# Performance work log

Measured on AMD Instinct MI355X. Metric: run time of the kernel, lower is better.

Reference implementation:

```python
import jax, jax.numpy as jnp
import numpy as np

K = 5          # kernel_size per dim
DIM = 2        # pseudo-coordinate dim
S = 2 ** DIM   # number of contributing knots for degree-1 B-spline
N = 50000
E = 800000
IN_C = 32
OUT_C = 64
NUM_LAYERS = 2
KPROD = K ** DIM  # 25 kernel weight matrices


def setup_inputs() -> dict:
    key = jax.random.key(0)
    ks = jax.random.split(key, 16)
    x = jax.random.normal(ks[0], (N, IN_C), dtype=jnp.float32)
    edge_index = jax.random.randint(ks[1], (2, E), 0, N, dtype=jnp.int64)
    edge_attr = jax.random.uniform(ks[2], (E, DIM), dtype=jnp.float32)
    inp = {"x": x, "edge_index": edge_index, "edge_attr": edge_attr}
    # SplineConv params per layer: spline weight [KPROD, in, out], root weight [in, out], bias [out]
    cin = IN_C
    for l in range(NUM_LAYERS):
        scale = 1.0 / np.sqrt(cin * S)
        inp[f"w{l}"] = jax.random.normal(ks[3 + 3 * l], (KPROD, cin, OUT_C), dtype=jnp.float32) * scale
        inp[f"root{l}"] = jax.random.normal(ks[4 + 3 * l], (cin, OUT_C), dtype=jnp.float32) / np.sqrt(cin)
        inp[f"b{l}"] = jnp.zeros((OUT_C,), dtype=jnp.float32)
        cin = OUT_C
    fin = IN_C + NUM_LAYERS * OUT_C  # 160, cat=True
    inp["fw"] = jax.random.normal(ks[10], (fin, OUT_C), dtype=jnp.float32) / np.sqrt(fin)
    inp["fb"] = jnp.zeros((OUT_C,), dtype=jnp.float32)
    return inp


def spline_basis(edge_attr):
    # degree-1 open B-spline over pseudo-coords in [0,1)
    v = edge_attr * (K - 1)                       # [E, DIM]
    bot = jnp.floor(v)
    frac = v - bot                                # [E, DIM]
    bits = ((jnp.arange(S)[:, None] >> jnp.arange(DIM)[None, :]) & 1)  # [S, DIM]
    bitsf = bits.astype(edge_attr.dtype)
    # basis_s = prod_d (frac_d if bit else 1-frac_d)
    basis = jnp.prod(bitsf[None] * frac[:, None, :] + (1.0 - bitsf[None]) * (1.0 - frac[:, None, :]), axis=-1)  # [E, S]
    kidx = jnp.clip(bot[:, None, :].astype(jnp.int32) + bits[None], 0, K - 1)  # [E, S, DIM]
    strides = (K ** jnp.arange(DIM)).astype(jnp.int32)
    widx = jnp.sum(kidx * strides[None, None, :], axis=-1)  # [E, S] in [0, KPROD)
    return basis, widx


def spline_conv(x, src, dst, basis, widx, w, root, b):
    # per-node, per-kernel transforms, then edge gather + basis weighting
    y = jnp.einsum('ni,kio->nko', x, w)           # [N, KPROD, out]
    msg = jnp.sum(basis[:, :, None] * y[src[:, None], widx], axis=1)  # [E, out]
    agg = jax.ops.segment_sum(msg, dst, num_segments=x.shape[0])
    deg = jax.ops.segment_sum(jnp.ones((src.shape[0],), x.dtype), dst, num_segments=x.shape[0])
    agg = agg / jnp.maximum(deg, 1.0)[:, None]    # mean aggregation
    return agg + x @ root + b


def reference(x, edge_index, edge_attr, w0, root0, b0, w1, root1, b1, fw, fb):
    src = edge_index[0].astype(jnp.int32)
    dst = edge_index[1].astype(jnp.int32)
    basis, widx = spline_basis(edge_attr)
    xs = [x]
    for w, root, b in ((w0, root0, b0), (w1, root1, b1)):
        xs.append(jax.nn.relu(spline_conv(xs[-1], src, dst, basis, widx, w, root, b)))
    h = jnp.concatenate(xs, axis=-1)              # cat=True -> [N, in + L*out]
    # dropout p=0.0 / eval mode -> identity
    return h @ fw + fb
```

## Files before the change

### kernel.cpp

```cpp
#include <hip/hip_runtime.h>
#include <hip/hip_bf16.h>
#include <hip/hip_fp16.h>


typedef __attribute__((ext_vector_type(8))) _Float16 f16x8;
typedef __attribute__((ext_vector_type(4))) _Float16 f16x4;
typedef __attribute__((ext_vector_type(4))) float f32x4;

constexpr int NN = 50000;
constexpr int EE = 800000;
constexpr int CHUNK = 256;
constexpr int EB = EE / 256;
static_assert(EE % 256 == 0, "prep grid assumes exact divisibility");
constexpr int ELIST_LEN = EE + 16 * CHUNK;
constexpr int NBLK_EDGE = ELIST_LEN / CHUNK;
constexpr int RT_BLK = (NN + 63) / 64;

__global__ __launch_bounds__(256) void detect_init(
    const long long* __restrict__ eidx, int* __restrict__ flag,
    int* __restrict__ degi) {
  if (blockIdx.x == 0 && threadIdx.x < 64) {
    long long v = eidx[threadIdx.x];
    bool ok = (v >= 0) && (v < (long long)NN);
    unsigned long long m = __ballot(ok);
    if (threadIdx.x == 0) flag[0] = (m == ~0ull) ? 1 : 0;
  }
  const int i = blockIdx.x * 256 + threadIdx.x;
  if (i < NN) degi[i] = 0;
}

constexpr int F2H_LEN8 = NN * 32 / 8;
constexpr int F2H_BLK = (F2H_LEN8 + 255) / 256;
constexpr int CW32_BLK = 4 * 16;
constexpr int CW64_BLK = 8 * 16;
constexpr int CFW_BLK = (64 * 160) / 256;
constexpr int CRT0_BLK = (64 * 32) / 256;
constexpr int CRT1_BLK = (64 * 64) / 256;
constexpr int CONV_BLK = F2H_BLK + CW32_BLK + CW64_BLK + CFW_BLK + CRT0_BLK + CRT1_BLK;

template <int IN>
__device__ __forceinline__ void conv_w_body(
    const float* __restrict__ w, _Float16* __restrict__ wcell, int c, int o) {
  constexpr int K = 4 * IN;
  constexpr int RS = K * 2;
  constexpr int OPR = K / 8;
  const int bx = c & 3, by = c >> 2;
  const int n = o / OPR;
  const int k0 = (o - n * OPR) * 8;
  const int ks = k0 >> 5;
  const int g2 = (k0 & 31) >> 3;
  const int s = (IN == 64) ? (ks & 3) : ks;
  const int i0 = ((IN == 64) ? (ks >> 2) * 32 : 0) + g2 * 8;
  const int kk = (bx + (s & 1)) + 5 * (by + (s >> 1));
  const float* wp = w + ((size_t)kk * IN + i0) * 64 + n;
  f16x8 v;
#pragma unroll
  for (int j = 0; j < 8; ++j) v[j] = (_Float16)wp[(size_t)j * 64];
  const int byte = n * RS + ((k0 * 2) ^ ((n & 15) << 4));
  *reinterpret_cast<f16x8*>(
      reinterpret_cast<char*>(wcell) + (size_t)c * (RS * 64) + byte) = v;
}

__global__ __launch_bounds__(256) void prep_conv(
    const void* __restrict__ eidx, const float* __restrict__ attr,
    const int* __restrict__ flag,
    int* __restrict__ src, int* __restrict__ dst, int* __restrict__ rankE,
    int* __restrict__ degi, int* __restrict__ bhT,
    const float* __restrict__ x0, const float* __restrict__ w0,
    const float* __restrict__ w1, const float* __restrict__ fw,
    const float* __restrict__ root0, const float* __restrict__ root1,
    _Float16* __restrict__ xh0, _Float16* __restrict__ wc0,
    _Float16* __restrict__ wc1, _Float16* __restrict__ fwT,
    _Float16* __restrict__ rt0T, _Float16* __restrict__ rt1T) {
  __shared__ int wc[4][16];
  const int tid = threadIdx.x;
  if (blockIdx.x < EB) {
    const int e = blockIdx.x * 256 + tid;
    int s, d;
    if (flag[0]) {
      s = (int)((const long long*)eidx)[e];
      d = (int)((const long long*)eidx)[EE + e];
    } else {
      s = ((const int*)eidx)[e];
      d = ((const int*)eidx)[EE + e];
    }
    src[e] = s;
    dst[e] = d;
    rankE[e] = atomicAdd(&degi[d], 1);
    const float v0 = attr[2 * e] * 4.0f, v1 = attr[2 * e + 1] * 4.0f;
    const int bx = min(max((int)floorf(v0), 0), 3);
    const int by = min(max((int)floorf(v1), 0), 3);
    const int c = bx + 4 * by;
    const int wave = tid >> 6, lane = tid & 63;
#pragma unroll
    for (int k = 0; k < 16; ++k) {
      unsigned long long mm = __ballot(c == k);
      if (lane == k) wc[wave][k] = __popcll(mm);
    }
    __syncthreads();
    if (tid < 16)
      bhT[tid * EB + blockIdx.x] = wc[0][tid] + wc[1][tid] + wc[2][tid] + wc[3][tid];
    return;
  }
  const int b = blockIdx.x - EB;
  if (b < F2H_BLK) {
    const int i = b * 256 + tid;
    if (i >= F2H_LEN8) return;
    const float4 a = reinterpret_cast<const float4*>(x0)[i * 2];
    const float4 bb = reinterpret_cast<const float4*>(x0)[i * 2 + 1];
    f16x8 v = {(_Float16)a.x, (_Float16)a.y, (_Float16)a.z, (_Float16)a.w,
               (_Float16)bb.x, (_Float16)bb.y, (_Float16)bb.z, (_Float16)bb.w};
    reinterpret_cast<f16x8*>(xh0)[i] = v;
  } else if (b < F2H_BLK + CW32_BLK) {
    const int r = b - F2H_BLK;
    conv_w_body<32>(w0, wc0, r >> 2, (r & 3) * 256 + tid);
  } else if (b < F2H_BLK + CW32_BLK + CW64_BLK) {
    const int r = b - F2H_BLK - CW32_BLK;
    conv_w_body<64>(w1, wc1, r >> 3, (r & 7) * 256 + tid);
  } else if (b < F2H_BLK + CW32_BLK + CW64_BLK + CFW_BLK) {
    const int i = (b - F2H_BLK - CW32_BLK - CW64_BLK) * 256 + tid;
    const int n = i / 160, k = i - n * 160;
    fwT[i] = (_Float16)fw[k * 64 + n];
  } else if (b < F2H_BLK + CW32_BLK + CW64_BLK + CFW_BLK + CRT0_BLK) {
    const int i = (b - F2H_BLK - CW32_BLK - CW64_BLK - CFW_BLK) * 256 + tid;
    const int n = i / 32, k = i - n * 32;
    rt0T[i] = (_Float16)root0[k * 64 + n];
  } else {
    const int i = (b - F2H_BLK - CW32_BLK - CW64_BLK - CFW_BLK - CRT0_BLK) * 256 + tid;
    const int n = i / 64, k = i - n * 64;
    rt1T[i] = (_Float16)root1[k * 64 + n];
  }
}

__global__ __launch_bounds__(1024) void scan_fused(
    const int* __restrict__ bhT, int* __restrict__ blkbaseT,
    int* __restrict__ chunkcell, int2* __restrict__ posrcS,
    const int* __restrict__ degi, int* __restrict__ dstbase) {
  const int wave = threadIdx.x >> 6, lane = threadIdx.x & 63;
  if (blockIdx.x == 0) {
    constexpr int CH = (EB + 63) / 64;
    __shared__ int ofs_s[16];
    __shared__ int tot_s[16];
    int v[CH];
#pragma unroll
    for (int ch = 0; ch < CH; ++ch) {
      const int b = ch * 64 + lane;
      v[ch] = (b < EB) ? bhT[wave * EB + b] : 0;
    }
    {
      int sum = 0;
#pragma unroll
      for (int ch = 0; ch < CH; ++ch) sum += v[ch];
#pragma unroll
      for (int off = 32; off > 0; off >>= 1) sum += __shfl_down(sum, off);
      if (lane == 0) tot_s[wave] = sum;
    }
    __syncthreads();
    if (threadIdx.x == 0) {
      int t = 0;
      for (int c = 0; c < 16; ++c) {
        ofs_s[c] = t;
        t += ((tot_s[c] + CHUNK - 1) / CHUNK) * CHUNK;
      }
    }
    __syncthreads();
    {
      const int nch = (tot_s[wave] + CHUNK - 1) / CHUNK;
      const int cb = ofs_s[wave] / CHUNK;
      for (int i = lane; i < nch; i += 64) chunkcell[cb + i] = wave;
      if (wave == 15) {
        const int totch = cb + nch;
        for (int i = totch + lane; i < NBLK_EDGE; i += 64) chunkcell[i] = -1;
      }
    }
    {
      const int startp = ofs_s[wave] + tot_s[wave];
      const int endp = ofs_s[wave] + ((tot_s[wave] + CHUNK - 1) / CHUNK) * CHUNK;
      for (int p = startp + lane; p < endp; p += 64) posrcS[p] = make_int2(-1, 0);
    }
    int running = ofs_s[wave];
#pragma unroll
    for (int ch = 0; ch < CH; ++ch) {
      int inc = v[ch];
#pragma unroll
      for (int off = 1; off < 64; off <<= 1) {
        int n = __shfl_up(inc, off);
        if (lane >= off) inc += n;
      }
      const int b = ch * 64 + lane;
      if (b < EB) blkbaseT[wave * EB + b] = running + inc - v[ch];
      running += __shfl(inc, 63);
    }
  } else {
    constexpr int SEG = NN / 16;
    constexpr int CH = (SEG + 63) / 64;
    __shared__ int wofs[16];
    const int nbase = wave * SEG;
    int v[CH];
#pragma unroll
    for (int ch = 0; ch < CH; ++ch) {
      const int i = ch * 64 + lane;
      v[ch] = (i < SEG) ? degi[nbase + i] : 0;
    }
    {
      int sum = 0;
#pragma unroll
      for (int ch = 0; ch < CH; ++ch) sum += v[ch];
#pragma unroll
      for (int off = 32; off > 0; off >>= 1) sum += __shfl_down(sum, off);
      if (lane == 0) wofs[wave] = sum;
    }
    __syncthreads();
    if (threadIdx.x == 0) {
      int t = 0;
      for (int w2 = 0; w2 < 16; ++w2) { int tv = wofs[w2]; wofs[w2] = t; t += tv; }
    }
    __syncthreads();
    int running = wofs[wave];
#pragma unroll
    for (int ch = 0; ch < CH; ++ch) {
      int inc = v[ch];
#pragma unroll
      for (int off = 1; off < 64; off <<= 1) {
        int n = __shfl_up(inc, off);
        if (lane >= off) inc += n;
      }
      const int i = ch * 64 + lane;
      if (i < SEG) dstbase[nbase + i] = running + inc - v[ch];
      running += __shfl(inc, 63);
    }
  }
}

__global__ __launch_bounds__(256) void scatter_edges(
    const float* __restrict__ attr, const int* __restrict__ blkbaseT,
    const int* __restrict__ srcArr, const int* __restrict__ dstArr,
    const int* __restrict__ rankE, const int* __restrict__ dstbase,
    int2* __restrict__ posrcS, f16x4* __restrict__ basS) {
  __shared__ int wc[4][16];
  __shared__ int bs[4][16];
  const int tid = threadIdx.x;
  const int e = blockIdx.x * 256 + tid;
  const float v0 = attr[2 * e] * 4.0f, v1 = attr[2 * e + 1] * 4.0f;
  const float fl0 = floorf(v0), fl1 = floorf(v1);
  const float fr0 = v0 - fl0, fr1 = v1 - fl1;
  const int bx = min(max((int)fl0, 0), 3);
  const int by = min(max((int)fl1, 0), 3);
  const int c = bx + 4 * by;
  const f16x4 bq = {(_Float16)((1.0f - fr0) * (1.0f - fr1)),
                    (_Float16)(fr0 * (1.0f - fr1)),
                    (_Float16)((1.0f - fr0) * fr1),
                    (_Float16)(fr0 * fr1)};
  const int wave = tid >> 6, lane = tid & 63;
  int rank = 0;
#pragma unroll
  for (int k = 0; k < 16; ++k) {
    unsigned long long mm = __ballot(c == k);
    if (k == c) rank = __popcll(mm & ((1ull << lane) - 1ull));
    if (lane == k) wc[wave][k] = __popcll(mm);
  }
  const int mypos = dstbase[dstArr[e]] + rankE[e];
  __syncthreads();
  if (tid < 16) {
    int running = blkbaseT[tid * EB + blockIdx.x];
#pragma unroll
    for (int w = 0; w < 4; ++w) { bs[w][tid] = running; running += wc[w][tid]; }
  }
  __syncthreads();
  const int p = bs[wave][c] + rank;
  posrcS[p] = make_int2(srcArr[e], mypos);
  basS[p] = bq;
}

template <int IN, bool TWOPASS>
__global__ __launch_bounds__(256) void edge_root(
    const _Float16* __restrict__ xh, const _Float16* __restrict__ wcell,
    const int* __restrict__ chunkcell,
    const int2* __restrict__ posrcS, const f16x4* __restrict__ basS,
    const _Float16* __restrict__ rootT, const float* __restrict__ bias,
    _Float16* __restrict__ rth,
    unsigned char* __restrict__ msg, float* __restrict__ agg) {
  constexpr int K = 4 * IN;
  constexpr int KSTEPS = K / 32;
  constexpr int RS = K * 2;
  constexpr int OPR = K / 8;
  constexpr int TILES = CHUNK / 64;
  constexpr int NCH = (IN == 64) ? 2 : 1;
  __shared__ f16x8 Wt[64 * OPR];
  const int tid = threadIdx.x;
  const int lane = tid & 63;
  const int wave = tid >> 6;
  const int g = lane >> 4, m = lane & 15;
  if (blockIdx.x >= NBLK_EDGE) {
    constexpr int KS = IN / 32;
    const int base = (blockIdx.x - NBLK_EDGE) * 64 + wave * 16;
    if (base >= NN) return;
    f16x8 bf[KS][4];
#pragma unroll
    for (int ks = 0; ks < KS; ++ks)
#pragma unroll
      for (int nt = 0; nt < 4; ++nt)
        bf[ks][nt] = *reinterpret_cast<const f16x8*>(
            rootT + (size_t)(nt * 16 + m) * IN + ks * 32 + g * 8);
    const int row = base + m;
    f16x8 a[KS];
#pragma unroll
    for (int ks = 0; ks < KS; ++ks)
      a[ks] = *reinterpret_cast<const f16x8*>(xh + (size_t)row * IN + ks * 32 + g * 8);
    f32x4 acc[4];
#pragma unroll
    for (int nt = 0; nt < 4; ++nt) {
      const float fv = bias[nt * 16 + m];
      acc[nt] = (f32x4){fv, fv, fv, fv};
    }
#pragma unroll
    for (int ks = 0; ks < KS; ++ks)
#pragma unroll
      for (int nt = 0; nt < 4; ++nt)
        acc[nt] = __builtin_amdgcn_mfma_f32_16x16x32_f16(a[ks], bf[ks][nt], acc[nt], 0, 0, 0);
#pragma unroll
    for (int r = 0; r < 4; ++r) {
      const int node = base + g * 4 + r;
      f16x4 pv = {(_Float16)acc[0][r], (_Float16)acc[1][r],
                  (_Float16)acc[2][r], (_Float16)acc[3][r]};
      *reinterpret_cast<f16x4*>(rth + (size_t)node * 64 + m * 4) = pv;
    }
    return;
  }
  const int c = chunkcell[blockIdx.x];
  if (c < 0) return;
  const int base = blockIdx.x * CHUNK;
  const int wbase = base + wave * (CHUNK / 4);
  int2 sp_t[TILES];
  f16x4 bas_t[TILES];
#pragma unroll
  for (int t = 0; t < TILES; ++t) sp_t[t] = posrcS[wbase + t * 16 + m];
#pragma unroll
  for (int t = 0; t < TILES; ++t) bas_t[t] = basS[wbase + t * 16 + m];
  {
    const f16x8* gw = reinterpret_cast<const f16x8*>(wcell) + (size_t)c * (64 * OPR);
    for (int o = tid; o < 64 * OPR; o += 256) Wt[o] = gw[o];
  }
  __syncthreads();
  f16x8 xc[TILES][NCH];
#pragma unroll
  for (int t = 0; t < TILES; ++t) {
    const int row = (sp_t[t].x >= 0) ? sp_t[t].x : 0;
    const f16x8* xr = reinterpret_cast<const f16x8*>(xh + (size_t)row * IN);
    xc[t][0] = xr[g];
    if constexpr (IN == 64) xc[t][1] = xr[4 + g];
  }
  f32x4 acc[TILES][4];
#pragma unroll
  for (int t = 0; t < TILES; ++t)
#pragma unroll
    for (int nt = 0; nt < 4; ++nt) acc[t][nt] = (f32x4){0.f, 0.f, 0.f, 0.f};
#pragma unroll
  for (int ks = 0; ks < KSTEPS; ++ks) {
    const int s = (IN == 64) ? (ks & 3) : ks;
    f16x8 a[TILES];
#pragma unroll
    for (int t = 0; t < TILES; ++t) {
      const f16x8 xin = (IN == 64 && (ks >> 2)) ? xc[t][1] : xc[t][0];
      a[t] = xin * bas_t[t][s];
    }
#pragma unroll
    for (int nt = 0; nt < 4; ++nt) {
      const int n = nt * 16 + m;
      const int byte = n * RS + (((ks * 64) + g * 16) ^ ((n & 15) << 4));
      const f16x8 bfrag = Wt[byte >> 4];
#pragma unroll
      for (int t = 0; t < TILES; ++t)
        acc[t][nt] = __builtin_amdgcn_mfma_f32_16x16x32_f16(a[t], bfrag, acc[t][nt], 0, 0, 0);
    }
  }
#pragma unroll
  for (int t = 0; t < TILES; ++t) {
#pragma unroll
    for (int r = 0; r < 4; ++r) {
      const int m2 = g * 4 + r;
      const int er = __shfl(sp_t[t].x, m2);
      const int pr = __shfl(sp_t[t].y, m2);
      if (er >= 0) {
        if constexpr (TWOPASS) {
          unsigned int p8 = __builtin_amdgcn_cvt_pk_fp8_f32(acc[t][0][r], acc[t][1][r], 0u, false);
          p8 = __builtin_amdgcn_cvt_pk_fp8_f32(acc[t][2][r], acc[t][3][r], p8, true);
          *reinterpret_cast<unsigned int*>(msg + (size_t)pr * 64 + m * 4) = p8;
        } else {
          float* ap = agg + (size_t)pr * 64 + m;
#pragma unroll
          for (int nt = 0; nt < 4; ++nt) atomicAdd(ap + nt * 16, acc[t][nt][r]);
        }
      }
    }
  }
}

__global__ __launch_bounds__(256) void pass2_kernel(
    const unsigned char* __restrict__ msg, const int* __restrict__ dstbase,
    const int* __restrict__ degi, const _Float16* __restrict__ rth,
    _Float16* __restrict__ xh_out) {
  const int wave = threadIdx.x >> 6, lane = threadIdx.x & 63;
  const int n = blockIdx.x * 4 + wave;
  const int q = lane >> 4, m = lane & 15;
  const _Float16 rv = rth[(size_t)n * 64 + m * 4 + q];
  const int b0 = dstbase[n], dg = degi[n];
  const unsigned int* mp =
      reinterpret_cast<const unsigned int*>(msg + (size_t)b0 * 64 + m * 4);
  float a0 = 0.f, a1 = 0.f, a2 = 0.f, a3 = 0.f;
  const int nfull = dg & ~15;
  int j0 = 0;
  for (; j0 < nfull; j0 += 16) {
    const unsigned int* bp = mp + (size_t)j0 * 16;
#pragma unroll
    for (int u = 0; u < 4; ++u) {
      const unsigned int pw = bp[(size_t)(u * 4 + q) * 16];
      const auto lo = __builtin_amdgcn_cvt_pk_f32_fp8(pw, false);
      const auto hi = __builtin_amdgcn_cvt_pk_f32_fp8(pw, true);
      a0 += lo[0]; a1 += lo[1]; a2 += hi[0]; a3 += hi[1];
    }
  }
  if (j0 < dg) {
#pragma unroll
    for (int u = 0; u < 4; ++u) {
      const int jj = j0 + u * 4 + q;
      const int jc = min(jj, dg - 1);
      const unsigned int pw = mp[(size_t)jc * 16];
      const auto lo = __builtin_amdgcn_cvt_pk_f32_fp8(pw, false);
      const auto hi = __builtin_amdgcn_cvt_pk_f32_fp8(pw, true);
      const float wv = (jj < dg) ? 1.0f : 0.0f;
      a0 = fmaf(wv, lo[0], a0);
      a1 = fmaf(wv, lo[1], a1);
      a2 = fmaf(wv, hi[0], a2);
      a3 = fmaf(wv, hi[1], a3);
    }
  }
  a0 += __shfl_xor(a0, 16); a0 += __shfl_xor(a0, 32);
  a1 += __shfl_xor(a1, 16); a1 += __shfl_xor(a1, 32);
  a2 += __shfl_xor(a2, 16); a2 += __shfl_xor(a2, 32);
  a3 += __shfl_xor(a3, 16); a3 += __shfl_xor(a3, 32);
  const float acc = (q == 0) ? a0 : (q == 1) ? a1 : (q == 2) ? a2 : a3;
  const float r = fmaxf(acc / fmaxf((float)dg, 1.0f) + (float)rv, 0.0f);
  xh_out[(size_t)n * 64 + lane] = (_Float16)r;
}

template <int IN>
__global__ __launch_bounds__(256) void finalize_kernel(
    const _Float16* __restrict__ xh_in, const float* __restrict__ agg,
    const int* __restrict__ degi, const float* __restrict__ root,
    const float* __restrict__ bias, _Float16* __restrict__ xh_out) {
  __shared__ float rl[IN * 64];
  for (int idx = threadIdx.x; idx < IN * 16; idx += 256)
    reinterpret_cast<float4*>(rl)[idx] = reinterpret_cast<const float4*>(root)[idx];
  __syncthreads();
  const int wave = threadIdx.x >> 6, lane = threadIdx.x & 63;
  const int n = blockIdx.x * 4 + wave;
  if (n >= NN) return;
  const float d = fmaxf((float)degi[n], 1.0f);
  float r = agg[(size_t)n * 64 + lane] / d + bias[lane];
  const _Float16* xr = xh_in + (size_t)n * IN;
#pragma unroll 8
  for (int i = 0; i < IN; ++i) r = fmaf((float)xr[i], rl[i * 64 + lane], r);
  r = fmaxf(r, 0.0f);
  xh_out[(size_t)n * 64 + lane] = (_Float16)r;
}

__global__ __launch_bounds__(256) void out_mfma(
    const _Float16* __restrict__ xh0, const _Float16* __restrict__ xh1,
    const _Float16* __restrict__ xh2, const _Float16* __restrict__ fwT,
    const float* __restrict__ fb, float* __restrict__ out) {
  const int lane = threadIdx.x & 63, wave = threadIdx.x >> 6;
  const int g = lane >> 4, m = lane & 15;
  const int base = blockIdx.x * 64 + wave * 16;
  if (base >= NN) return;
  f16x8 bf[5][4];
#pragma unroll
  for (int ks = 0; ks < 5; ++ks)
#pragma unroll
    for (int nt = 0; nt < 4; ++nt)
      bf[ks][nt] = *reinterpret_cast<const f16x8*>(
          fwT + (size_t)(nt * 16 + m) * 160 + ks * 32 + g * 8);
  const int row = base + m;
  f16x8 a[5];
  a[0] = *reinterpret_cast<const f16x8*>(xh0 + (size_t)row * 32 + g * 8);
  a[1] = *reinterpret_cast<const f16x8*>(xh1 + (size_t)row * 64 + g * 8);
  a[2] = *reinterpret_cast<const f16x8*>(xh1 + (size_t)row * 64 + 32 + g * 8);
  a[3] = *reinterpret_cast<const f16x8*>(xh2 + (size_t)row * 64 + g * 8);
  a[4] = *reinterpret_cast<const f16x8*>(xh2 + (size_t)row * 64 + 32 + g * 8);
  f32x4 acc[4];
#pragma unroll
  for (int nt = 0; nt < 4; ++nt) {
    const float fv = fb[nt * 16 + m];
    acc[nt] = (f32x4){fv, fv, fv, fv};
  }
#pragma unroll
  for (int ks = 0; ks < 5; ++ks)
#pragma unroll
    for (int nt = 0; nt < 4; ++nt)
      acc[nt] = __builtin_amdgcn_mfma_f32_16x16x32_f16(a[ks], bf[ks][nt], acc[nt], 0, 0, 0);
#pragma unroll
  for (int r = 0; r < 4; ++r) {
    float* op = out + (size_t)(base + g * 4 + r) * 64 + m;
#pragma unroll
    for (int nt = 0; nt < 4; ++nt) op[nt * 16] = acc[nt][r];
  }
}

extern "C" void kernel_launch(void* const* d_in, const int* in_sizes, int n_in,
                              void* d_out, int out_size, void* d_ws, size_t ws_size,
                              hipStream_t stream) {
  const float* x0 = (const float*)d_in[0];
  const void* eidx = d_in[1];
  const float* attr = (const float*)d_in[2];
  const float* w0 = (const float*)d_in[3];
  const float* root0 = (const float*)d_in[4];
  const float* b0 = (const float*)d_in[5];
  const float* w1 = (const float*)d_in[6];
  const float* root1 = (const float*)d_in[7];
  const float* b1 = (const float*)d_in[8];
  const float* fw = (const float*)d_in[9];
  const float* fb = (const float*)d_in[10];
  float* out = (float*)d_out;
  (void)in_sizes; (void)n_in; (void)out_size;

  char* wsb = (char*)d_ws;
  size_t off = 0;
  auto alloc = [&](size_t bytes) -> void* {
    void* p = wsb + off;
    off += (bytes + 255) & ~(size_t)255;
    return p;
  };
  int* flag = (int*)alloc(256);
  int* src = (int*)alloc(sizeof(int) * EE);
  int* dst = (int*)alloc(sizeof(int) * EE);
  int* rankE = (int*)alloc(sizeof(int) * EE);
  int2* posrcS = (int2*)alloc(sizeof(int2) * ELIST_LEN);
  f16x4* basS = (f16x4*)alloc(sizeof(f16x4) * ELIST_LEN);
  int* chunkcell = (int*)alloc(sizeof(int) * NBLK_EDGE);
  int* degi = (int*)alloc(sizeof(int) * NN);
  int* dstbase = (int*)alloc(sizeof(int) * NN);
  int* bhT = (int*)alloc(sizeof(int) * EB * 16);
  int* blkbaseT = (int*)alloc(sizeof(int) * EB * 16);
  _Float16* xh0 = (_Float16*)alloc(sizeof(_Float16) * NN * 32);
  _Float16* xh1 = (_Float16*)alloc(sizeof(_Float16) * NN * 64);
  _Float16* xh2 = (_Float16*)alloc(sizeof(_Float16) * NN * 64);
  _Float16* rth = (_Float16*)alloc(sizeof(_Float16) * NN * 64);
  _Float16* wc0 = (_Float16*)alloc(sizeof(_Float16) * 16 * 128 * 64);
  _Float16* wc1 = (_Float16*)alloc(sizeof(_Float16) * 16 * 256 * 64);
  _Float16* fwT = (_Float16*)alloc(sizeof(_Float16) * 64 * 160);
  _Float16* rt0T = (_Float16*)alloc(sizeof(_Float16) * 64 * 32);
  _Float16* rt1T = (_Float16*)alloc(sizeof(_Float16) * 64 * 64);
  const size_t common = off;
  const bool twopass = ws_size >= common + (size_t)EE * 64;
  unsigned char* msg = nullptr;
  float* agg = nullptr;
  if (twopass) msg = (unsigned char*)alloc((size_t)EE * 64);
  else         agg = (float*)alloc(sizeof(float) * (size_t)NN * 64);

  detect_init<<<(NN + 255) / 256, 256, 0, stream>>>(
      (const long long*)eidx, flag, degi);
  prep_conv<<<EB + CONV_BLK, 256, 0, stream>>>(
      eidx, attr, flag, src, dst, rankE, degi, bhT,
      x0, w0, w1, fw, root0, root1, xh0, wc0, wc1, fwT, rt0T, rt1T);
  scan_fused<<<2, 1024, 0, stream>>>(bhT, blkbaseT, chunkcell, posrcS, degi, dstbase);
  scatter_edges<<<EB, 256, 0, stream>>>(attr, blkbaseT, src, dst, rankE, dstbase,
                                        posrcS, basS);

  if (twopass) {
    edge_root<32, true><<<NBLK_EDGE + RT_BLK, 256, 0, stream>>>(
        xh0, wc0, chunkcell, posrcS, basS, rt0T, b0, rth, msg, nullptr);
    pass2_kernel<<<NN / 4, 256, 0, stream>>>(msg, dstbase, degi, rth, xh1);
    edge_root<64, true><<<NBLK_EDGE + RT_BLK, 256, 0, stream>>>(
        xh1, wc1, chunkcell, posrcS, basS, rt1T, b1, rth, msg, nullptr);
    pass2_kernel<<<NN / 4, 256, 0, stream>>>(msg, dstbase, degi, rth, xh2);
  } else {
    hipMemsetAsync(agg, 0, sizeof(float) * NN * 64, stream);
    edge_root<32, false><<<NBLK_EDGE, 256, 0, stream>>>(
        xh0, wc0, chunkcell, posrcS, basS, rt0T, b0, rth, nullptr, agg);
    finalize_kernel<32><<<(NN + 3) / 4, 256, 0, stream>>>(xh0, agg, degi, root0, b0, xh1);
    hipMemsetAsync(agg, 0, sizeof(float) * NN * 64, stream);
    edge_root<64, false><<<NBLK_EDGE, 256, 0, stream>>>(
        xh1, wc1, chunkcell, posrcS, basS, rt1T, b1, rth, nullptr, agg);
    finalize_kernel<64><<<(NN + 3) / 4, 256, 0, stream>>>(xh1, agg, degi, root1, b1, xh2);
  }

  out_mfma<<<(NN + 63) / 64, 256, 0, stream>>>(xh0, xh1, xh2, fwT, fb, out);
}
```

Measured before the change: 185.7 us.

## Fuse second-layer aggregation with output GEMM and double edge chunk per block

```diff
diff --git a/kernel.cpp b/kernel.cpp
--- a/kernel.cpp
+++ b/kernel.cpp
@@ -9,11 +9,11 @@
 
 constexpr int NN = 50000;
 constexpr int EE = 800000;
-constexpr int CHUNK = 256;
+constexpr int BCHUNK = 512;
 constexpr int EB = EE / 256;
 static_assert(EE % 256 == 0, "prep grid assumes exact divisibility");
-constexpr int ELIST_LEN = EE + 16 * CHUNK;
-constexpr int NBLK_EDGE = ELIST_LEN / CHUNK;
+constexpr int ELIST_LEN = EE + 16 * BCHUNK;
+constexpr int NBLK_EDGE = ELIST_LEN / BCHUNK + 1;
 constexpr int RT_BLK = (NN + 63) / 64;
 
 __global__ __launch_bounds__(256) void detect_init(
@@ -160,13 +160,13 @@
       int t = 0;
       for (int c = 0; c < 16; ++c) {
         ofs_s[c] = t;
-        t += ((tot_s[c] + CHUNK - 1) / CHUNK) * CHUNK;
+        t += ((tot_s[c] + BCHUNK - 1) / BCHUNK) * BCHUNK;
       }
     }
     __syncthreads();
     {
-      const int nch = (tot_s[wave] + CHUNK - 1) / CHUNK;
-      const int cb = ofs_s[wave] / CHUNK;
+      const int nch = (tot_s[wave] + BCHUNK - 1) / BCHUNK;
+      const int cb = ofs_s[wave] / BCHUNK;
       for (int i = lane; i < nch; i += 64) chunkcell[cb + i] = wave;
       if (wave == 15) {
         const int totch = cb + nch;
@@ -175,7 +175,7 @@
     }
     {
       const int startp = ofs_s[wave] + tot_s[wave];
-      const int endp = ofs_s[wave] + ((tot_s[wave] + CHUNK - 1) / CHUNK) * CHUNK;
+      const int endp = ofs_s[wave] + ((tot_s[wave] + BCHUNK - 1) / BCHUNK) * BCHUNK;
       for (int p = startp + lane; p < endp; p += 64) posrcS[p] = make_int2(-1, 0);
     }
     int running = ofs_s[wave];
@@ -284,7 +284,7 @@
   constexpr int KSTEPS = K / 32;
   constexpr int RS = K * 2;
   constexpr int OPR = K / 8;
-  constexpr int TILES = CHUNK / 64;
+  constexpr int TILES = 4;
   constexpr int NCH = (IN == 64) ? 2 : 1;
   __shared__ f16x8 Wt[64 * OPR];
   const int tid = threadIdx.x;
@@ -329,82 +329,78 @@
   }
   const int c = chunkcell[blockIdx.x];
   if (c < 0) return;
-  const int base = blockIdx.x * CHUNK;
-  const int wbase = base + wave * (CHUNK / 4);
-  int2 sp_t[TILES];
-  f16x4 bas_t[TILES];
-#pragma unroll
-  for (int t = 0; t < TILES; ++t) sp_t[t] = posrcS[wbase + t * 16 + m];
-#pragma unroll
-  for (int t = 0; t < TILES; ++t) bas_t[t] = basS[wbase + t * 16 + m];
+  const int base = blockIdx.x * BCHUNK;
   {
     const f16x8* gw = reinterpret_cast<const f16x8*>(wcell) + (size_t)c * (64 * OPR);
     for (int o = tid; o < 64 * OPR; o += 256) Wt[o] = gw[o];
   }
   __syncthreads();
-  f16x8 xc[TILES][NCH];
-#pragma unroll
-  for (int t = 0; t < TILES; ++t) {
-    const int row = (sp_t[t].x >= 0) ? sp_t[t].x : 0;
-    const f16x8* xr = reinterpret_cast<const f16x8*>(xh + (size_t)row * IN);
-    xc[t][0] = xr[g];
-    if constexpr (IN == 64) xc[t][1] = xr[4 + g];
-  }
-  f32x4 acc[TILES][4];
-#pragma unroll
-  for (int t = 0; t < TILES; ++t)
-#pragma unroll
-    for (int nt = 0; nt < 4; ++nt) acc[t][nt] = (f32x4){0.f, 0.f, 0.f, 0.f};
-#pragma unroll
-  for (int ks = 0; ks < KSTEPS; ++ks) {
-    const int s = (IN == 64) ? (ks & 3) : ks;
-    f16x8 a[TILES];
+#pragma unroll 1
+  for (int rd = 0; rd < 2; ++rd) {
+    const int wbase = base + rd * 256 + wave * 64;
+    int2 sp_t[TILES];
+    f16x4 bas_t[TILES];
+#pragma unroll
+    for (int t = 0; t < TILES; ++t) sp_t[t] = posrcS[wbase + t * 16 + m];
+#pragma unroll
+    for (int t = 0; t < TILES; ++t) bas_t[t] = basS[wbase + t * 16 + m];
+    f16x8 xc[TILES][NCH];
 #pragma unroll
     for (int t = 0; t < TILES; ++t) {
-      const f16x8 xin = (IN == 64 && (ks >> 2)) ? xc[t][1] : xc[t][0];
-      a[t] = xin * bas_t[t][s];
-    }
-#pragma unroll
-    for (int nt = 0; nt < 4; ++nt) {
-      const int n = nt * 16 + m;
-      const int byte = n * RS + (((ks * 64) + g * 16) ^ ((n & 15) << 4));
-      const f16x8 bfrag = Wt[byte >> 4];
-#pragma unroll
-      for (int t = 0; t < TILES; ++t)
-        acc[t][nt] = __builtin_amdgcn_mfma_f32_16x16x32_f16(a[t], bfrag, acc[t][nt], 0, 0, 0);
-    }
-  }
-#pragma unroll
-  for (int t = 0; t < TILES; ++t) {
-#pragma unroll
-    for (int r = 0; r < 4; ++r) {
-      const int m2 = g * 4 + r;
-      const int er = __shfl(sp_t[t].x, m2);
-      const int pr = __shfl(sp_t[t].y, m2);
-      if (er >= 0) {
-        if constexpr (TWOPASS) {
-          unsigned int p8 = __builtin_amdgcn_cvt_pk_fp8_f32(acc[t][0][r], acc[t][1][r], 0u, false);
-          p8 = __builtin_amdgcn_cvt_pk_fp8_f32(acc[t][2][r], acc[t][3][r], p8, true);
-          *reinterpret_cast<unsigned int*>(msg + (size_t)pr * 64 + m * 4) = p8;
-        } else {
-          float* ap = agg + (size_t)pr * 64 + m;
-#pragma unroll
-          for (int nt = 0; nt < 4; ++nt) atomicAdd(ap + nt * 16, acc[t][nt][r]);
+      const int row = (sp_t[t].x >= 0) ? sp_t[t].x : 0;
+      const f16x8* xr = reinterpret_cast<const f16x8*>(xh + (size_t)row * IN);
+      xc[t][0] = xr[g];
+      if constexpr (IN == 64) xc[t][1] = xr[4 + g];
+    }
+    f32x4 acc[TILES][4];
+#pragma unroll
+    for (int t = 0; t < TILES; ++t)
+#pragma unroll
+      for (int nt = 0; nt < 4; ++nt) acc[t][nt] = (f32x4){0.f, 0.f, 0.f, 0.f};
+#pragma unroll
+    for (int ks = 0; ks < KSTEPS; ++ks) {
+      const int s = (IN == 64) ? (ks & 3) : ks;
+      f16x8 a[TILES];
+#pragma unroll
+      for (int t = 0; t < TILES; ++t) {
+        const f16x8 xin = (IN == 64 && (ks >> 2)) ? xc[t][1] : xc[t][0];
+        a[t] = xin * bas_t[t][s];
+      }
+#pragma unroll
+      for (int nt = 0; nt < 4; ++nt) {
+        const int n = nt * 16 + m;
+        const int byte = n * RS + (((ks * 64) + g * 16) ^ ((n & 15) << 4));
+        const f16x8 bfrag = Wt[byte >> 4];
+#pragma unroll
+        for (int t = 0; t < TILES; ++t)
+          acc[t][nt] = __builtin_amdgcn_mfma_f32_16x16x32_f16(a[t], bfrag, acc[t][nt], 0, 0, 0);
+      }
+    }
+#pragma unroll
+    for (int t = 0; t < TILES; ++t) {
+#pragma unroll
+      for (int r = 0; r < 4; ++r) {
+        const int m2 = g * 4 + r;
+        const int er = __shfl(sp_t[t].x, m2);
+        const int pr = __shfl(sp_t[t].y, m2);
+        if (er >= 0) {
+          if constexpr (TWOPASS) {
+            unsigned int p8 = __builtin_amdgcn_cvt_pk_fp8_f32(acc[t][0][r], acc[t][1][r], 0u, false);
+            p8 = __builtin_amdgcn_cvt_pk_fp8_f32(acc[t][2][r], acc[t][3][r], p8, true);
+            *reinterpret_cast<unsigned int*>(msg + (size_t)pr * 64 + m * 4) = p8;
+          } else {
+            float* ap = agg + (size_t)pr * 64 + m;
+#pragma unroll
+            for (int nt = 0; nt < 4; ++nt) atomicAdd(ap + nt * 16, acc[t][nt][r]);
+          }
         }
       }
     }
   }
 }
 
-__global__ __launch_bounds__(256) void pass2_kernel(
-    const unsigned char* __restrict__ msg, const int* __restrict__ dstbase,
-    const int* __restrict__ degi, const _Float16* __restrict__ rth,
-    _Float16* __restrict__ xh_out) {
-  const int wave = threadIdx.x >> 6, lane = threadIdx.x & 63;
-  const int n = blockIdx.x * 4 + wave;
-  const int q = lane >> 4, m = lane & 15;
-  const _Float16 rv = rth[(size_t)n * 64 + m * 4 + q];
-  const int b0 = dstbase[n], dg = degi[n];
+__device__ __forceinline__ float seg_reduce_fp8(
+    const unsigned char* __restrict__ msg, int b0, int dg, int q, int m) {
   const unsigned int* mp =
       reinterpret_cast<const unsigned int*>(msg + (size_t)b0 * 64 + m * 4);
   float a0 = 0.f, a1 = 0.f, a2 = 0.f, a3 = 0.f;
@@ -439,9 +435,63 @@
   a1 += __shfl_xor(a1, 16); a1 += __shfl_xor(a1, 32);
   a2 += __shfl_xor(a2, 16); a2 += __shfl_xor(a2, 32);
   a3 += __shfl_xor(a3, 16); a3 += __shfl_xor(a3, 32);
-  const float acc = (q == 0) ? a0 : (q == 1) ? a1 : (q == 2) ? a2 : a3;
-  const float r = fmaxf(acc / fmaxf((float)dg, 1.0f) + (float)rv, 0.0f);
+  return (q == 0) ? a0 : (q == 1) ? a1 : (q == 2) ? a2 : a3;
+}
+
+__global__ __launch_bounds__(256) void pass2_kernel(
+    const unsigned char* __restrict__ msg, const int* __restrict__ dstbase,
+    const int* __restrict__ degi, const _Float16* __restrict__ rth,
+    _Float16* __restrict__ xh_out) {
+  const int wave = threadIdx.x >> 6, lane = threadIdx.x & 63;
+  const int n = blockIdx.x * 4 + wave;
+  const int q = lane >> 4, m = lane & 15;
+  const _Float16 rv = rth[(size_t)n * 64 + m * 4 + q];
+  const float acc = seg_reduce_fp8(msg, dstbase[n], degi[n], q, m);
+  const float r = fmaxf(acc / fmaxf((float)degi[n], 1.0f) + (float)rv, 0.0f);
   xh_out[(size_t)n * 64 + lane] = (_Float16)r;
+}
+
+__global__ __launch_bounds__(256) void pass2_out(
+    const unsigned char* __restrict__ msg, const int* __restrict__ dstbase,
+    const int* __restrict__ degi, const _Float16* __restrict__ rth,
+    const _Float16* __restrict__ xh0, const _Float16* __restrict__ xh1,
+    const _Float16* __restrict__ fwT, const float* __restrict__ fb,
+    float* __restrict__ out) {
+  __shared__ _Float16 sh[16][72];
+  const int wave = threadIdx.x >> 6, lane = threadIdx.x & 63;
+  const int q = lane >> 4, m = lane & 15;
+  const int n0 = blockIdx.x * 16;
+#pragma unroll 1
+  for (int i = 0; i < 4; ++i) {
+    const int nl = wave * 4 + i;
+    const int n = n0 + nl;
+    const _Float16 rv = rth[(size_t)n * 64 + m * 4 + q];
+    const float acc = seg_reduce_fp8(msg, dstbase[n], degi[n], q, m);
+    const float r = fmaxf(acc / fmaxf((float)degi[n], 1.0f) + (float)rv, 0.0f);
+    sh[nl][lane] = (_Float16)r;
+  }
+  __syncthreads();
+  const int g = lane >> 4;
+  const int col = wave * 16 + m;
+  f16x8 bf[5];
+#pragma unroll
+  for (int ks = 0; ks < 5; ++ks)
+    bf[ks] = *reinterpret_cast<const f16x8*>(fwT + (size_t)col * 160 + ks * 32 + g * 8);
+  const int row = n0 + m;
+  f16x8 a[5];
+  a[0] = *reinterpret_cast<const f16x8*>(xh0 + (size_t)row * 32 + g * 8);
+  a[1] = *reinterpret_cast<const f16x8*>(xh1 + (size_t)row * 64 + g * 8);
+  a[2] = *reinterpret_cast<const f16x8*>(xh1 + (size_t)row * 64 + 32 + g * 8);
+  a[3] = *reinterpret_cast<const f16x8*>(&sh[m][g * 8]);
+  a[4] = *reinterpret_cast<const f16x8*>(&sh[m][32 + g * 8]);
+  const float fv = fb[col];
+  f32x4 acc = (f32x4){fv, fv, fv, fv};
+#pragma unroll
+  for (int ks = 0; ks < 5; ++ks)
+    acc = __builtin_amdgcn_mfma_f32_16x16x32_f16(a[ks], bf[ks], acc, 0, 0, 0);
+#pragma unroll
+  for (int r = 0; r < 4; ++r)
+    out[(size_t)(n0 + g * 4 + r) * 64 + col] = acc[r];
 }
 
 template <int IN>
@@ -572,7 +622,8 @@
     pass2_kernel<<<NN / 4, 256, 0, stream>>>(msg, dstbase, degi, rth, xh1);
     edge_root<64, true><<<NBLK_EDGE + RT_BLK, 256, 0, stream>>>(
         xh1, wc1, chunkcell, posrcS, basS, rt1T, b1, rth, msg, nullptr);
-    pass2_kernel<<<NN / 4, 256, 0, stream>>>(msg, dstbase, degi, rth, xh2);
+    pass2_out<<<NN / 16, 256, 0, stream>>>(msg, dstbase, degi, rth,
+                                           xh0, xh1, fwT, fb, out);
   } else {
     hipMemsetAsync(agg, 0, sizeof(float) * NN * 64, stream);
     edge_root<32, false><<<NBLK_EDGE, 256, 0, stream>>>(
@@ -582,7 +633,6 @@
     edge_root<64, false><<<NBLK_EDGE, 256, 0, stream>>>(
         xh1, wc1, chunkcell, posrcS, basS, rt1T, b1, rth, nullptr, agg);
     finalize_kernel<64><<<(NN + 3) / 4, 256, 0, stream>>>(xh1, agg, degi, root1, b1, xh2);
-  }
-
-  out_mfma<<<(NN + 63) / 64, 256, 0, stream>>>(xh0, xh1, xh2, fwT, fb, out);
-}
+    out_mfma<<<(NN + 63) / 64, 256, 0, stream>>>(xh0, xh1, xh2, fwT, fb, out);
+  }
+}
```

After: 220.5 us. 18.7% more time.
